# Optimization experiments

Hardware: AMD Instinct MI355X
Metric: run time of the kernel (lower is better)

Reference implementation:

```python
import jax, jax.numpy as jnp
import numpy as np

H, DK, DV, SEG, D = 16, 64, 64, 512, 1024


def setup_inputs() -> dict:
    key = jax.random.key(0)
    ks = jax.random.split(key, 6)
    B, T = 2, 8192
    x = jax.random.normal(ks[0], (B, T, D), jnp.float32)
    Wq = jax.random.normal(ks[1], (H * DK, D), jnp.float32) * 0.02
    Wk = jax.random.normal(ks[2], (H * DK, D), jnp.float32) * 0.02
    Wv = jax.random.normal(ks[3], (H * DV, D), jnp.float32) * 0.02
    Wout = jax.random.normal(ks[4], (D, H * DV), jnp.float32) * 0.02
    betas = jax.random.normal(ks[5], (1, H, 1, DV), jnp.float32)
    return {"x": x, "Wq": Wq, "Wk": Wk, "Wv": Wv, "Wout": Wout, "betas": betas}


def reference(x, Wq, Wk, Wv, Wout, betas):
    B, T, _ = x.shape
    n_seg = T // SEG
    # Projections for the whole sequence, then PyTorch-style .view head split:
    # per segment, (B, SEG, H*dk).view(B, H, SEG, dk) is a raw row-major reshape.
    q = (x @ Wq.T).reshape(B, n_seg, H, SEG, DK)
    k = (x @ Wk.T).reshape(B, n_seg, H, SEG, DK)
    v = (x @ Wv.T).reshape(B, n_seg, H, SEG, DV)
    qs = jnp.moveaxis(q, 1, 0)  # (n_seg, B, H, SEG, DK)
    ks_ = jnp.moveaxis(k, 1, 0)
    vs = jnp.moveaxis(v, 1, 0)

    gate = jax.nn.sigmoid(betas)                 # (1, H, 1, DV)
    scale = 1.0 / jnp.sqrt(jnp.float32(DK))

    mem0 = jnp.zeros((B, H, DK, DV), x.dtype)
    # z broadcasts from (B,H,DV,1) to (B,H,DV,DK) on first update; start dense.
    z0 = jnp.zeros((B, H, DV, DK), x.dtype)

    def step(carry, seg):
        mem, z = carry
        q, k, v = seg
        sq = jax.nn.elu(q) + 1.0                 # (B,H,S,DK)
        sk = jax.nn.elu(k) + 1.0
        z = z + sk.sum(axis=-2, keepdims=True)   # (B,H,DV,DK) via broadcast
        scores = jnp.einsum('bhsd,bhtd->bhst', q, k) * scale
        att_dot = jnp.einsum('bhst,bhtv->bhsv', jax.nn.softmax(scores, axis=-1), v)
        att_mem = jnp.einsum('bhsd,bhdv->bhsv', sq, mem) / jnp.einsum('bhsd,bhdv->bhsv', sq, z)
        mem = mem + jnp.einsum('bhsd,bhsv->bhdv', sk, v)  # linear update (after att_mem)
        att = gate * att_mem + (1.0 - gate) * att_dot     # (B,H,S,DV)
        # PyTorch .view(B, SEG, H*DV) on (B,H,S,DV): raw reshape, no transpose.
        y = att.reshape(B, SEG, H * DV) @ Wout.T          # (B,SEG,D)
        return (mem, z), y

    (_, _), ys = jax.lax.scan(step, (mem0, z0), (qs, ks_, vs))
    out = jnp.moveaxis(ys, 0, 1).reshape(B, T, D)
    return out
```

## Files before the change

kernel.cpp:

```cpp
#include <hip/hip_runtime.h>


#define H_ 16
#define SEG_ 512
#define NSEG_ 16
#define B_ 2
#define T_ 8192
#define D_ 1024
#define BT_ 16384

#define NPROJ ((size_t)BT_ * D_)
#define NW ((size_t)D_ * D_)

__device__ unsigned short g_qb[NPROJ], g_kb[NPROJ], g_vb[NPROJ];
__device__ unsigned short g_xh[NPROJ];
__device__ unsigned short g_wqkv[3 * NW];
__device__ unsigned short g_ath[NPROJ], g_atl[NPROJ];
__device__ unsigned short g_woh[NW], g_wol[NW];
__device__ unsigned short g_vt[(size_t)512 * 64 * 512];
__device__ float g_M[(size_t)512 * 4096];
__device__ float g_z[(size_t)512 * 64];

typedef __attribute__((ext_vector_type(8))) short short8;
typedef __attribute__((ext_vector_type(8))) unsigned short ushort8;
typedef __attribute__((ext_vector_type(4))) float f32x4;

__device__ __forceinline__ float elu1(float x) {
    return x > 0.f ? x + 1.f : __expf(x);
}
__device__ __forceinline__ unsigned short f2bf(float x) {
    unsigned u = __float_as_uint(x);
    u += 0x7fffu + ((u >> 16) & 1u);
    return (unsigned short)(u >> 16);
}
__device__ __forceinline__ float bf2f(unsigned short h) {
    return __uint_as_float((unsigned)h << 16);
}
__device__ __forceinline__ void load_lds16(const unsigned short* g, unsigned short* l) {
    __builtin_amdgcn_global_load_lds(
        (const __attribute__((address_space(1))) unsigned int*)g,
        (__attribute__((address_space(3))) unsigned int*)l, 16, 0, 0);
}
__device__ __forceinline__ int sz8(int row, int blk) {
    return row * 64 + ((blk ^ (row & 7)) << 3);
}

__global__ __launch_bounds__(256) void prep_cast(
    const float* __restrict__ x, const float* __restrict__ Wq,
    const float* __restrict__ Wk, const float* __restrict__ Wv,
    const float* __restrict__ Wout,
    unsigned short* __restrict__ xh, unsigned short* __restrict__ wqkv,
    unsigned short* __restrict__ woh, unsigned short* __restrict__ wol)
{
    const int b = blockIdx.x;
    const int nXB = (int)(NPROJ / 1024);
    const int nWB = (int)(NW / 1024);
    if (b < nXB + 3 * nWB) {
        const float* in;
        unsigned short* out;
        int i;
        if (b < nXB) {
            in = x; out = xh; i = (b * 256 + threadIdx.x) * 4;
        } else {
            const int wsel = (b - nXB) / nWB;
            const int wb   = (b - nXB) % nWB;
            in  = wsel == 0 ? Wq : (wsel == 1 ? Wk : Wv);
            out = wqkv + (size_t)wsel * NW;
            i = (wb * 256 + threadIdx.x) * 4;
        }
        float4 v = *(const float4*)(in + i);
        ushort4 h;
        h.x = f2bf(v.x); h.y = f2bf(v.y); h.z = f2bf(v.z); h.w = f2bf(v.w);
        *(ushort4*)(out + i) = h;
    } else {
        const int wb = b - nXB - 3 * nWB;
        const int i = (wb * 256 + threadIdx.x) * 4;
        float4 v = *(const float4*)(Wout + i);
        ushort4 h, l;
        h.x = f2bf(v.x); l.x = f2bf(v.x - bf2f(h.x));
        h.y = f2bf(v.y); l.y = f2bf(v.y - bf2f(h.y));
        h.z = f2bf(v.z); l.z = f2bf(v.z - bf2f(h.z));
        h.w = f2bf(v.w); l.w = f2bf(v.w - bf2f(h.w));
        *(ushort4*)(woh + i) = h;
        *(ushort4*)(wol + i) = l;
    }
}


#define VMC(N) asm volatile("s_waitcnt vmcnt(" #N ")" ::: "memory")

#define STAGE_A(p, h, tt, u) \
    load_lds16(Aw + ((h) * 128 + (u) * 8) * 1024 + (tt) * 64, \
               &lds[(p) * 32768 + ((h) * 128 + w * 16 + (u) * 8) * 64])
#define STAGE_B(p, h, tt, u) \
    load_lds16(Bww + ((h) * 128 + (u) * 8) * 1024 + (tt) * 64, \
               &lds[(p) * 32768 + 16384 + ((h) * 128 + w * 16 + (u) * 8) * 64])
#define STAGE_AH(p, h, tt) do { STAGE_A(p, h, tt, 0); STAGE_A(p, h, tt, 1); } while (0)
#define STAGE_BH(p, h, tt) do { STAGE_B(p, h, tt, 0); STAGE_B(p, h, tt, 1); } while (0)

#define LDA(PBUF, MLO) do { \
    _Pragma("unroll") for (int m2 = 0; m2 < 4; ++m2) \
    _Pragma("unroll") for (int ks2 = 0; ks2 < 2; ++ks2) \
        a[m2][ks2] = *(const short8*)&lds[(PBUF) * 32768 + aoff[ks2] + ((MLO) + m2) * 1024]; \
} while (0)

#define LDB(PBUF) do { \
    _Pragma("unroll") for (int n2 = 0; n2 < 4; ++n2) \
    _Pragma("unroll") for (int ks2 = 0; ks2 < 2; ++ks2) \
        b[n2][ks2] = *(const short8*)&lds[(PBUF) * 32768 + boff[ks2] + n2 * 1024]; \
} while (0)

#define MFMA_QUAD(MLO, NLO) do { \
    _Pragma("unroll") for (int m2 = 0; m2 < 4; ++m2) \
    _Pragma("unroll") for (int n2 = 0; n2 < 2; ++n2) \
    _Pragma("unroll") for (int ks2 = 0; ks2 < 2; ++ks2) \
        acc[(MLO) + m2][(NLO) + n2] = __builtin_amdgcn_mfma_f32_16x16x32_bf16( \
            a[m2][ks2], b[(NLO) + n2][ks2], acc[(MLO) + m2][(NLO) + n2], 0, 0, 0); \
} while (0)

#define PH(MLO, NLO) do { \
    __builtin_amdgcn_s_barrier(); \
    asm volatile("s_waitcnt lgkmcnt(0)" ::: "memory"); \
    __builtin_amdgcn_sched_barrier(0); \
    __builtin_amdgcn_s_setprio(1); \
    MFMA_QUAD(MLO, NLO); \
    __builtin_amdgcn_s_setprio(0); \
    __builtin_amdgcn_sched_barrier(0); \
    __builtin_amdgcn_s_barrier(); \
} while (0)

__global__ __launch_bounds__(512, 2) void gemm_qkv8(
    const unsigned short* __restrict__ A, const unsigned short* __restrict__ Bw,
    unsigned short* __restrict__ Q, unsigned short* __restrict__ Kp,
    unsigned short* __restrict__ V)
{
    __shared__ unsigned short lds[65536];
    const int t = threadIdx.x, lane = t & 63, w = t >> 6;
    const int wave_m = w >> 2, wave_n = w & 3;

    const int bid = blockIdx.x;
    const int sb = (bid & 7) * 96 + (bid >> 3);
    const int mb = sb / 12, nb = sb % 12;
    const int m0 = mb * 256, n0 = nb * 256;

    const int lrow = lane >> 3;
    const int lcol = ((lane & 7) ^ lrow) * 8;
    const unsigned short* Aw  = A  + (size_t)(m0 + w * 16 + lrow) * 1024 + lcol;
    const unsigned short* Bww = Bw + (size_t)(n0 + w * 16 + lrow) * 1024 + lcol;

    const int fr = lane & 15, g4 = lane >> 4;
    int aoff[2], boff[2];
#pragma unroll
    for (int ks2 = 0; ks2 < 2; ++ks2) {
        aoff[ks2] = (wave_m * 128 + fr) * 64 + (((ks2 * 4 + g4) ^ (fr & 7)) * 8);
        boff[ks2] = 16384 + (wave_n * 64 + fr) * 64 + (((ks2 * 4 + g4) ^ (fr & 7)) * 8);
    }

    f32x4 acc[8][4];
#pragma unroll
    for (int i = 0; i < 8; ++i)
#pragma unroll
        for (int j = 0; j < 4; ++j) acc[i][j] = (f32x4)0.f;
    short8 a[4][2], b[4][2];

    STAGE_BH(0, 0, 0); STAGE_BH(0, 1, 0); STAGE_AH(0, 0, 0); STAGE_AH(0, 1, 0);
    STAGE_BH(1, 0, 1); STAGE_BH(1, 1, 1); STAGE_AH(1, 0, 1);
    VMC(6);
    __builtin_amdgcn_s_barrier();

#pragma unroll 1
    for (int it = 0; it < 7; ++it) {
        const int t1 = 2 * it + 1, t2 = 2 * it + 2, t3 = 2 * it + 3;
        LDB(0); LDA(0, 0);
        STAGE_AH(1, 1, t1);
        PH(0, 0);
        STAGE_BH(0, 0, t2);
        PH(0, 2);
        LDA(0, 4);
        STAGE_BH(0, 1, t2);
        PH(4, 0);
        STAGE_AH(0, 0, t2);
        VMC(6);
        PH(4, 2);
        LDB(1); LDA(1, 0);
        STAGE_AH(0, 1, t2);
        PH(0, 0);
        STAGE_BH(1, 0, t3);
        PH(0, 2);
        LDA(1, 4);
        STAGE_BH(1, 1, t3);
        PH(4, 0);
        STAGE_AH(1, 0, t3);
        VMC(6);
        PH(4, 2);
    }
    LDB(0); LDA(0, 0);
    STAGE_AH(1, 1, 15);
    PH(0, 0);
    PH(0, 2);
    LDA(0, 4);
    PH(4, 0);
    VMC(0);
    PH(4, 2);
    LDB(1); LDA(1, 0);
    PH(0, 0);
    PH(0, 2);
    LDA(1, 4);
    PH(4, 0);
    PH(4, 2);

    const int ccol = lane & 15, crow = (lane >> 4) * 4;
#pragma unroll
    for (int m = 0; m < 8; ++m)
#pragma unroll
        for (int n = 0; n < 4; ++n) {
            const int col = wave_n * 64 + n * 16 + ccol;
            const int cb = col >> 3, cl = col & 7;
#pragma unroll
            for (int r = 0; r < 4; ++r) {
                const int row = wave_m * 128 + m * 16 + crow + r;
                lds[row * 256 + ((cb ^ (row & 31)) << 3) + cl] = f2bf(acc[m][n][r]);
            }
        }
    __syncthreads();
    const int which = n0 >> 10, col0 = n0 & 1023;
    unsigned short* outp = which == 0 ? Q : (which == 1 ? Kp : V);
    const int orow = t >> 1, och = (t & 1) * 128;
    unsigned short* gp = outp + (size_t)(m0 + orow) * 1024 + col0 + och;
#pragma unroll
    for (int u = 0; u < 128; u += 8) {
        const int bo = (och + u) >> 3;
        *(ushort8*)(gp + u) = *(const ushort8*)&lds[orow * 256 + ((bo ^ (orow & 31)) << 3)];
    }
}


#define OSTG(p, arrp, aroff, tt, u) \
    load_lds16(arrp + (size_t)(u) * 16 * 1024 + (tt) * 32, \
               &lds[(p) * 32768 + (aroff) + (w * 32 + (u) * 16) * 32])
#define OUNIT(p, arrp, aroff, tt) do { OSTG(p, arrp, aroff, tt, 0); OSTG(p, arrp, aroff, tt, 1); } while (0)

#define OLDA(PBUF, MLO) do { \
    _Pragma("unroll") for (int m2 = 0; m2 < 4; ++m2) { \
        ah[m2] = *(const short8*)&lds[(PBUF) * 32768 +         ao + ((MLO) + m2) * 512]; \
        al[m2] = *(const short8*)&lds[(PBUF) * 32768 +  8192 + ao + ((MLO) + m2) * 512]; \
    } \
} while (0)

#define OLDB(PBUF) do { \
    _Pragma("unroll") for (int n2 = 0; n2 < 4; ++n2) { \
        bh[n2] = *(const short8*)&lds[(PBUF) * 32768 + 16384 + bo + n2 * 512]; \
        bl[n2] = *(const short8*)&lds[(PBUF) * 32768 + 24576 + bo + n2 * 512]; \
    } \
} while (0)

#define OQUAD(MLO, NLO) do { \
    _Pragma("unroll") for (int m2 = 0; m2 < 4; ++m2) \
    _Pragma("unroll") for (int n2 = 0; n2 < 2; ++n2) { \
        acc[(MLO) + m2][(NLO) + n2] = __builtin_amdgcn_mfma_f32_16x16x32_bf16( \
            ah[m2], bh[(NLO) + n2], acc[(MLO) + m2][(NLO) + n2], 0, 0, 0); \
        acc[(MLO) + m2][(NLO) + n2] = __builtin_amdgcn_mfma_f32_16x16x32_bf16( \
            al[m2], bh[(NLO) + n2], acc[(MLO) + m2][(NLO) + n2], 0, 0, 0); \
        acc[(MLO) + m2][(NLO) + n2] = __builtin_amdgcn_mfma_f32_16x16x32_bf16( \
            ah[m2], bl[(NLO) + n2], acc[(MLO) + m2][(NLO) + n2], 0, 0, 0); \
    } \
} while (0)

#define OPH(MLO, NLO) do { \
    __builtin_amdgcn_s_barrier(); \
    asm volatile("s_waitcnt lgkmcnt(0)" ::: "memory"); \
    __builtin_amdgcn_sched_barrier(0); \
    __builtin_amdgcn_s_setprio(1); \
    OQUAD(MLO, NLO); \
    __builtin_amdgcn_s_setprio(0); \
    __builtin_amdgcn_sched_barrier(0); \
    __builtin_amdgcn_s_barrier(); \
} while (0)

__global__ __launch_bounds__(512, 2) void gemm_bt8(
    const unsigned short* __restrict__ Ah, const unsigned short* __restrict__ Al,
    const unsigned short* __restrict__ Bh, const unsigned short* __restrict__ Bl,
    float* __restrict__ C)
{
    __shared__ unsigned short lds[65536];
    const int t = threadIdx.x, lane = t & 63, w = t >> 6;
    const int wave_m = w >> 2, wave_n = w & 3;

    const int bid = blockIdx.x;
    const int sb = (bid & 7) * 32 + (bid >> 3);
    const int m0 = (sb >> 2) * 256, n0 = (sb & 3) * 256;

    const int lrow = lane >> 2;
    const int lcol = ((lane & 3) ^ ((lane >> 3) & 3)) * 8;
    const unsigned short* Ahp = Ah + (size_t)(m0 + w * 32 + lrow) * 1024 + lcol;
    const unsigned short* Alp = Al + (size_t)(m0 + w * 32 + lrow) * 1024 + lcol;
    const unsigned short* Bhp = Bh + (size_t)(n0 + w * 32 + lrow) * 1024 + lcol;
    const unsigned short* Blp = Bl + (size_t)(n0 + w * 32 + lrow) * 1024 + lcol;

    const int fr = lane & 15, g4 = lane >> 4;
    const int xo = (g4 ^ ((fr >> 1) & 3)) * 8;
    const int ao = (wave_m * 128 + fr) * 32 + xo;
    const int bo = (wave_n * 64 + fr) * 32 + xo;

    f32x4 acc[8][4];
#pragma unroll
    for (int i = 0; i < 8; ++i)
#pragma unroll
        for (int j = 0; j < 4; ++j) acc[i][j] = (f32x4)0.f;
    short8 ah[4], al[4], bh[4], bl[4];

    OUNIT(0, Bhp, 16384, 0); OUNIT(0, Blp, 24576, 0); OUNIT(0, Ahp, 0, 0); OUNIT(0, Alp, 8192, 0);
    OUNIT(1, Bhp, 16384, 1); OUNIT(1, Blp, 24576, 1); OUNIT(1, Ahp, 0, 1);
    VMC(6);
    __builtin_amdgcn_s_barrier();

#pragma unroll 1
    for (int it = 0; it < 15; ++it) {
        const int t1 = 2 * it + 1, t2 = 2 * it + 2, t3 = 2 * it + 3;
        OLDB(0); OLDA(0, 0);
        OUNIT(1, Alp, 8192, t1);
        OPH(0, 0);
        OUNIT(0, Bhp, 16384, t2);
        OPH(0, 2);
        OLDA(0, 4);
        OUNIT(0, Blp, 24576, t2);
        OPH(4, 0);
        OUNIT(0, Ahp, 0, t2);
        VMC(6);
        OPH(4, 2);
        OLDB(1); OLDA(1, 0);
        OUNIT(0, Alp, 8192, t2);
        OPH(0, 0);
        OUNIT(1, Bhp, 16384, t3);
        OPH(0, 2);
        OLDA(1, 4);
        OUNIT(1, Blp, 24576, t3);
        OPH(4, 0);
        OUNIT(1, Ahp, 0, t3);
        VMC(6);
        OPH(4, 2);
    }
    OLDB(0); OLDA(0, 0);
    OUNIT(1, Alp, 8192, 31);
    OPH(0, 0);
    OPH(0, 2);
    OLDA(0, 4);
    OPH(4, 0);
    VMC(0);
    OPH(4, 2);
    OLDB(1); OLDA(1, 0);
    OPH(0, 0);
    OPH(0, 2);
    OLDA(1, 4);
    OPH(4, 0);
    OPH(4, 2);

    const int ccol = lane & 15, crow = (lane >> 4) * 4;
#pragma unroll
    for (int m = 0; m < 8; ++m)
#pragma unroll
        for (int n = 0; n < 4; ++n) {
            float* cp = C + (size_t)(m0 + wave_m * 128 + m * 16 + crow) * 1024
                          + (n0 + wave_n * 64 + n * 16 + ccol);
#pragma unroll
            for (int r = 0; r < 4; ++r) cp[(size_t)r * 1024] = acc[m][n][r];
        }
}

__global__ __launch_bounds__(256) void seg_stats(
    const unsigned short* __restrict__ kproj, const unsigned short* __restrict__ vproj,
    float* __restrict__ Mseg, float* __restrict__ zsum,
    unsigned short* __restrict__ vtg)
{
    __shared__ unsigned short sm_kh[64 * 64];
    __shared__ unsigned short sm_kl[64 * 64];
    __shared__ unsigned short sm_vt[64 * 64];
    const int idx = blockIdx.x;
    const int seg = idx & 15;
    const int bh  = idx >> 4;
    const int h   = bh & 15;
    const int b   = bh >> 4;
    const size_t base = ((size_t)b * T_ + (size_t)seg * SEG_ + (size_t)h * 32) * D_;
    const unsigned short* kt = kproj + base;
    const unsigned short* vt = vproj + base;
    const int t    = threadIdx.x;
    const int lane = t & 63;
    const int w    = t >> 6;
    const int c16  = lane & 15;
    const int g4   = lane >> 4;
    const int lr   = t >> 2;
    const int lc   = (t & 3) * 16;

    short8 bones;
#pragma unroll
    for (int j = 0; j < 8; ++j) bones[j] = (short)0x3F80;

    f32x4 acc[4];
#pragma unroll
    for (int nt = 0; nt < 4; ++nt) acc[nt] = (f32x4)0.f;
    f32x4 zacc = (f32x4)0.f;

    for (int c0 = 0; c0 < SEG_; c0 += 64) {
        __syncthreads();
        {
            const int row = c0 + lane;
            const unsigned short* kp = kt + (size_t)row * 64 + w * 16;
            const unsigned short* vp = vt + (size_t)row * 64 + w * 16;
            ushort8 k0 = *(const ushort8*)kp, k1 = *(const ushort8*)(kp + 8);
            ushort8 v0 = *(const ushort8*)vp, v1 = *(const ushort8*)(vp + 8);
            const int tb = lane >> 3, tl = lane & 7;
#pragma unroll
            for (int e = 0; e < 8; ++e) {
                const float f0 = elu1(bf2f(k0[e]));
                const unsigned short h0 = f2bf(f0), l0 = f2bf(f0 - bf2f(h0));
                const float f1 = elu1(bf2f(k1[e]));
                const unsigned short h1 = f2bf(f1), l1 = f2bf(f1 - bf2f(h1));
                const int a0 = sz8(w * 16 + e,     tb) + tl;
                const int a1 = sz8(w * 16 + 8 + e, tb) + tl;
                sm_kh[a0] = h0; sm_kl[a0] = l0; sm_vt[a0] = v0[e];
                sm_kh[a1] = h1; sm_kl[a1] = l1; sm_vt[a1] = v1[e];
            }
        }
        __syncthreads();
#pragma unroll
        for (int ks = 0; ks < 2; ++ks) {
            const short8 ahh = *(const short8*)&sm_kh[sz8(w * 16 + c16, ks * 4 + g4)];
            const short8 alo = *(const short8*)&sm_kl[sz8(w * 16 + c16, ks * 4 + g4)];
            zacc = __builtin_amdgcn_mfma_f32_16x16x32_bf16(ahh, bones, zacc, 0, 0, 0);
            zacc = __builtin_amdgcn_mfma_f32_16x16x32_bf16(alo, bones, zacc, 0, 0, 0);
#pragma unroll
            for (int nt = 0; nt < 4; ++nt) {
                const short8 bv = *(const short8*)&sm_vt[sz8(nt * 16 + c16, ks * 4 + g4)];
                acc[nt] = __builtin_amdgcn_mfma_f32_16x16x32_bf16(ahh, bv, acc[nt], 0, 0, 0);
                acc[nt] = __builtin_amdgcn_mfma_f32_16x16x32_bf16(alo, bv, acc[nt], 0, 0, 0);
            }
        }
        {
            unsigned short* vo = vtg + ((size_t)idx * 64 + lr) * 512 + c0 + lc;
            *(ushort8*)vo       = *(const ushort8*)&sm_vt[sz8(lr, lc >> 3)];
            *(ushort8*)(vo + 8) = *(const ushort8*)&sm_vt[sz8(lr, (lc >> 3) + 1)];
        }
    }
    float* Mout = Mseg + (size_t)idx * 4096;
#pragma unroll
    for (int nt = 0; nt < 4; ++nt)
#pragma unroll
        for (int r = 0; r < 4; ++r)
            Mout[(size_t)(w * 16 + g4 * 4 + r) * 64 + nt * 16 + c16] = acc[nt][r];
    if (c16 == 0) {
#pragma unroll
        for (int r = 0; r < 4; ++r)
            zsum[(size_t)idx * 64 + w * 16 + g4 * 4 + r] = zacc[r];
    }
}

__global__ __launch_bounds__(256) void prefix_scan(
    float* __restrict__ M, float* __restrict__ z)
{
    const int blk = blockIdx.x;
    const int bh  = blk >> 2, sl = blk & 3;
    const int t   = threadIdx.x;
    const size_t off = (size_t)bh * NSEG_ * 4096 + (size_t)sl * 1024 + (size_t)t * 4;
    float4 run = make_float4(0.f, 0.f, 0.f, 0.f);
    float runz = 0.f;
    for (int seg = 0; seg < NSEG_; ++seg) {
        const size_t o = off + (size_t)seg * 4096;
        float4 m = *(const float4*)(M + o);
        *(float4*)(M + o) = run;
        run.x += m.x; run.y += m.y; run.z += m.z; run.w += m.w;
        if (sl == 0 && t < 64) {
            const size_t oz = ((size_t)bh * NSEG_ + seg) * 64 + t;
            runz += z[oz];
            z[oz] = runz;
        }
    }
}

__global__ __launch_bounds__(512) void attn_mfma(
    const unsigned short* __restrict__ qproj, const unsigned short* __restrict__ kproj,
    const unsigned short* __restrict__ vtg, const float* __restrict__ memb,
    const float* __restrict__ Zaf, const float* __restrict__ betas,
    unsigned short* __restrict__ ath, unsigned short* __restrict__ atl)
{
    __shared__ unsigned short smK[8 * 4096];
    __shared__ unsigned short smV[8 * 4096];
    __shared__ unsigned short smM[4096];
    __shared__ unsigned short smP[128 * 64];
    __shared__ float Zsh[64], gsh[64];

    const int rest = blockIdx.x;
    const int bh   = rest >> 4;
    const int seg  = rest & 15;
    const int h    = bh & 15;
    const int b    = bh >> 4;
    const size_t base = ((size_t)b * T_ + (size_t)seg * SEG_ + (size_t)h * 32) * D_;

    const int t    = threadIdx.x;
    const int lane = t & 63;
    const int w    = t >> 6;
    const int c16  = lane & 15;
    const int g4   = lane >> 4;
    const int sr   = t >> 3;
    const int sg   = t & 7;

    const unsigned short* qt = qproj + base;
    const unsigned short* kt = kproj + base;
    const unsigned short* vt = vtg + (size_t)rest * (64 * 512);
    const float* mb = memb + (size_t)rest * 4096;

    if (t < 64) {
        Zsh[t] = Zaf[(size_t)rest * 64 + t];
        gsh[t] = 1.f / (1.f + __expf(-betas[h * 64 + t]));
    }

    {
        const float* mp = mb + (size_t)sr * 64 + sg * 8;
#pragma unroll
        for (int u = 0; u < 2; ++u) {
            float4 m4 = *(const float4*)(mp + u * 4);
            smM[sz8(sg * 8 + u * 4 + 0, sr >> 3) + (sr & 7)] = f2bf(m4.x);
            smM[sz8(sg * 8 + u * 4 + 1, sr >> 3) + (sr & 7)] = f2bf(m4.y);
            smM[sz8(sg * 8 + u * 4 + 2, sr >> 3) + (sr & 7)] = f2bf(m4.z);
            smM[sz8(sg * 8 + u * 4 + 3, sr >> 3) + (sr & 7)] = f2bf(m4.w);
        }
    }
#pragma unroll
    for (int kb = 0; kb < 8; ++kb) {
        *(ushort8*)&smK[kb * 4096 + sz8(sr, sg)] =
            *(const ushort8*)(kt + (size_t)(kb * 64 + sr) * 64 + sg * 8);
        *(ushort8*)&smV[kb * 4096 + sz8(sr, sg)] =
            *(const ushort8*)(vt + (size_t)sr * 512 + kb * 64 + sg * 8);
    }
    __syncthreads();

    short8 bones;
#pragma unroll
    for (int j = 0; j < 8; ++j) bones[j] = (short)0x3F80;

#pragma unroll 1
    for (int qc2 = 0; qc2 < 4; ++qc2) {
        short8 qh[2], sqh[2];
        float rowsum = 0.f;
#pragma unroll
        for (int ks = 0; ks < 2; ++ks) {
            const unsigned short* qp =
                qt + (size_t)(qc2 * 128 + w * 16 + c16) * 64 + g4 * 8 + ks * 32;
            ushort8 qv = *(const ushort8*)qp;
            short8 qf, sf;
#pragma unroll
            for (int j = 0; j < 8; ++j) {
                float e = elu1(bf2f(qv[j]));
                rowsum += e;
                qf[j] = (short)qv[j];
                sf[j] = (short)f2bf(e);
            }
            qh[ks] = qf; sqh[ks] = sf;
        }
        rowsum += __shfl_xor(rowsum, 16);
        rowsum += __shfl_xor(rowsum, 32);

        f32x4 numf[4];
#pragma unroll
        for (int nf = 0; nf < 4; ++nf) numf[nf] = (f32x4)0.f;
#pragma unroll
        for (int ks = 0; ks < 2; ++ks)
#pragma unroll
            for (int nf = 0; nf < 4; ++nf) {
                short8 bm = *(const short8*)&smM[sz8(nf * 16 + c16, g4 + ks * 4)];
                numf[nf] = __builtin_amdgcn_mfma_f32_16x16x32_bf16(sqh[ks], bm, numf[nf], 0, 0, 0);
            }

        f32x4 o[4];
#pragma unroll
        for (int nf = 0; nf < 4; ++nf) o[nf] = (f32x4)0.f;
        float mrow[4] = {-1e30f, -1e30f, -1e30f, -1e30f};
        float lrow[4] = {0.f, 0.f, 0.f, 0.f};

#pragma unroll 1
        for (int kb = 0; kb < 8; ++kb) {
            f32x4 s[4];
#pragma unroll
            for (int nf = 0; nf < 4; ++nf) s[nf] = (f32x4)0.f;
#pragma unroll
            for (int ks = 0; ks < 2; ++ks)
#pragma unroll
                for (int nf = 0; nf < 4; ++nf) {
                    short8 bk = *(const short8*)&smK[kb * 4096 + sz8(nf * 16 + c16, g4 + ks * 4)];
                    s[nf] = __builtin_amdgcn_mfma_f32_16x16x32_bf16(qh[ks], bk, s[nf], 0, 0, 0);
                }
#pragma unroll
            for (int nf = 0; nf < 4; ++nf) s[nf] *= 0.125f;

            float pmax[4];
#pragma unroll
            for (int r = 0; r < 4; ++r)
                pmax[r] = fmaxf(fmaxf(s[0][r], s[1][r]), fmaxf(s[2][r], s[3][r]));
            const bool ok = pmax[0] <= mrow[0] + 8.f && pmax[1] <= mrow[1] + 8.f &&
                            pmax[2] <= mrow[2] + 8.f && pmax[3] <= mrow[3] + 8.f;
            if (!__all(ok)) {
#pragma unroll
                for (int r = 0; r < 4; ++r) {
                    float mx = pmax[r];
                    mx = fmaxf(mx, __shfl_xor(mx, 1));
                    mx = fmaxf(mx, __shfl_xor(mx, 2));
                    mx = fmaxf(mx, __shfl_xor(mx, 4));
                    mx = fmaxf(mx, __shfl_xor(mx, 8));
                    const float mnew = fmaxf(mrow[r], mx);
                    const float corr = __expf(mrow[r] - mnew);
                    mrow[r] = mnew;
                    lrow[r] *= corr;
#pragma unroll
                    for (int nf = 0; nf < 4; ++nf) o[nf][r] *= corr;
                }
            }
#pragma unroll
            for (int nf = 0; nf < 4; ++nf)
#pragma unroll
                for (int r = 0; r < 4; ++r) {
                    s[nf][r] = __expf(s[nf][r] - mrow[r]);
                    smP[sz8(w * 16 + g4 * 4 + r, nf * 2 + (c16 >> 3)) + (c16 & 7)] =
                        f2bf(s[nf][r]);
                }

            f32x4 psum = (f32x4)0.f;
#pragma unroll
            for (int ks = 0; ks < 2; ++ks) {
                short8 pa = *(const short8*)&smP[sz8(w * 16 + c16, g4 + ks * 4)];
                psum = __builtin_amdgcn_mfma_f32_16x16x32_bf16(pa, bones, psum, 0, 0, 0);
#pragma unroll
                for (int nf = 0; nf < 4; ++nf) {
                    short8 bv = *(const short8*)&smV[kb * 4096 + sz8(nf * 16 + c16, g4 + ks * 4)];
                    o[nf] = __builtin_amdgcn_mfma_f32_16x16x32_bf16(pa, bv, o[nf], 0, 0, 0);
                }
            }
#pragma unroll
            for (int r = 0; r < 4; ++r) lrow[r] += psum[r];
        }

        float rs[4], invl[4];
#pragma unroll
        for (int r = 0; r < 4; ++r) {
            rs[r]   = __shfl(rowsum, (g4 << 2) + r);
            invl[r] = 1.f / lrow[r];
        }
        float res[4][4];
#pragma unroll
        for (int nf = 0; nf < 4; ++nf) {
            const int col = nf * 16 + c16;
            const float Zc = Zsh[col], gc = gsh[col];
            const float izc = 1.f / Zc;
#pragma unroll
            for (int r = 0; r < 4; ++r) {
                const float adot = o[nf][r] * invl[r];
                const float amem = numf[nf][r] * izc / rs[r];
                res[nf][r] = gc * amem + (1.f - gc) * adot;
            }
        }
        const int orow = t >> 2, olc = (t & 3) * 16;
        const size_t ob = base + (size_t)(qc2 * 128 + orow) * 64 + olc;
#pragma unroll
        for (int nf = 0; nf < 4; ++nf)
#pragma unroll
            for (int r = 0; r < 4; ++r)
                smP[sz8(w * 16 + g4 * 4 + r, nf * 2 + (c16 >> 3)) + (c16 & 7)] =
                    f2bf(res[nf][r]);
        __syncthreads();
        *(ushort8*)(ath + ob)     = *(const ushort8*)&smP[sz8(orow, olc >> 3)];
        *(ushort8*)(ath + ob + 8) = *(const ushort8*)&smP[sz8(orow, (olc >> 3) + 1)];
        __syncthreads();
#pragma unroll
        for (int nf = 0; nf < 4; ++nf)
#pragma unroll
            for (int r = 0; r < 4; ++r) {
                const unsigned short hv = f2bf(res[nf][r]);
                smP[sz8(w * 16 + g4 * 4 + r, nf * 2 + (c16 >> 3)) + (c16 & 7)] =
                    f2bf(res[nf][r] - bf2f(hv));
            }
        __syncthreads();
        *(ushort8*)(atl + ob)     = *(const ushort8*)&smP[sz8(orow, olc >> 3)];
        *(ushort8*)(atl + ob + 8) = *(const ushort8*)&smP[sz8(orow, (olc >> 3) + 1)];
        __syncthreads();
    }
}

extern "C" void kernel_launch(void* const* d_in, const int* in_sizes, int n_in,
                              void* d_out, int out_size, void* d_ws, size_t ws_size,
                              hipStream_t stream) {
    const float* x     = (const float*)d_in[0];
    const float* Wq    = (const float*)d_in[1];
    const float* Wk    = (const float*)d_in[2];
    const float* Wv    = (const float*)d_in[3];
    const float* Wout  = (const float*)d_in[4];
    const float* betas = (const float*)d_in[5];
    float* out = (float*)d_out;
    (void)d_ws; (void)ws_size;

    float *M, *z;
    unsigned short *qb, *kb, *vb, *xh, *wqkv, *vt, *ath, *atl, *woh, *wol;
    hipGetSymbolAddress((void**)&qb,   HIP_SYMBOL(g_qb));
    hipGetSymbolAddress((void**)&kb,   HIP_SYMBOL(g_kb));
    hipGetSymbolAddress((void**)&vb,   HIP_SYMBOL(g_vb));
    hipGetSymbolAddress((void**)&xh,   HIP_SYMBOL(g_xh));
    hipGetSymbolAddress((void**)&wqkv, HIP_SYMBOL(g_wqkv));
    hipGetSymbolAddress((void**)&vt,   HIP_SYMBOL(g_vt));
    hipGetSymbolAddress((void**)&ath,  HIP_SYMBOL(g_ath));
    hipGetSymbolAddress((void**)&atl,  HIP_SYMBOL(g_atl));
    hipGetSymbolAddress((void**)&woh,  HIP_SYMBOL(g_woh));
    hipGetSymbolAddress((void**)&wol,  HIP_SYMBOL(g_wol));
    hipGetSymbolAddress((void**)&M,    HIP_SYMBOL(g_M));
    hipGetSymbolAddress((void**)&z,    HIP_SYMBOL(g_z));

    const int nXB = (int)(NPROJ / 1024), nWB = (int)(NW / 1024);
    prep_cast<<<nXB + 4 * nWB, 256, 0, stream>>>(x, Wq, Wk, Wv, Wout,
                                                 xh, wqkv, woh, wol);

    gemm_qkv8<<<dim3(768), 512, 0, stream>>>(xh, wqkv, qb, kb, vb);
    seg_stats<<<B_ * H_ * NSEG_, 256, 0, stream>>>(kb, vb, M, z, vt);
    prefix_scan<<<B_ * H_ * 4, 256, 0, stream>>>(M, z);
    attn_mfma<<<B_ * H_ * NSEG_, 512, 0, stream>>>(qb, kb, vt, M, z, betas, ath, atl);
    gemm_bt8<<<dim3(256), 512, 0, stream>>>(ath, atl, woh, wol, out);
}
```

Measured before the change: 483.7 us.

## Halve QKV GEMM LDS tile K-depth to raise occupancy and split epilogue

Cuts the QKV projection GEMM's per-stage K slice from 64 to 32, which halves LDS use from 128KB to 64KB and doubles the main-loop iteration count. Launch bounds rise from 2 to 4 blocks per CU, and the epilogue writes the 256-row output tile in two 128-row halves so it fits the smaller LDS. The goal is more resident blocks to hide latency, at the cost of more barriers and shallower prefetch per stage. The output GEMM's shared array is renamed with no functional change.

```diff
diff --git a/kernel.cpp b/kernel.cpp
--- a/kernel.cpp
+++ b/kernel.cpp
@@ -89,33 +89,28 @@
 
 #define VMC(N) asm volatile("s_waitcnt vmcnt(" #N ")" ::: "memory")
 
-#define STAGE_A(p, h, tt, u) \
-    load_lds16(Aw + ((h) * 128 + (u) * 8) * 1024 + (tt) * 64, \
-               &lds[(p) * 32768 + ((h) * 128 + w * 16 + (u) * 8) * 64])
-#define STAGE_B(p, h, tt, u) \
-    load_lds16(Bww + ((h) * 128 + (u) * 8) * 1024 + (tt) * 64, \
-               &lds[(p) * 32768 + 16384 + ((h) * 128 + w * 16 + (u) * 8) * 64])
-#define STAGE_AH(p, h, tt) do { STAGE_A(p, h, tt, 0); STAGE_A(p, h, tt, 1); } while (0)
-#define STAGE_BH(p, h, tt) do { STAGE_B(p, h, tt, 0); STAGE_B(p, h, tt, 1); } while (0)
+#define QSTG_A(p, u, tt) \
+    load_lds16(Aw + (size_t)(u) * 128 * 1024 + (tt) * 32, \
+               &lds[(p) * 16384 + (u) * 4096 + w * 512])
+#define QSTG_B(p, u, tt) \
+    load_lds16(Bww + (size_t)(u) * 128 * 1024 + (tt) * 32, \
+               &lds[(p) * 16384 + 8192 + (u) * 4096 + w * 512])
 
 #define LDA(PBUF, MLO) do { \
     _Pragma("unroll") for (int m2 = 0; m2 < 4; ++m2) \
-    _Pragma("unroll") for (int ks2 = 0; ks2 < 2; ++ks2) \
-        a[m2][ks2] = *(const short8*)&lds[(PBUF) * 32768 + aoff[ks2] + ((MLO) + m2) * 1024]; \
+        a[m2] = *(const short8*)&lds[(PBUF) * 16384 + aoff + ((MLO) + m2) * 512]; \
 } while (0)
 
 #define LDB(PBUF) do { \
     _Pragma("unroll") for (int n2 = 0; n2 < 4; ++n2) \
-    _Pragma("unroll") for (int ks2 = 0; ks2 < 2; ++ks2) \
-        b[n2][ks2] = *(const short8*)&lds[(PBUF) * 32768 + boff[ks2] + n2 * 1024]; \
+        b[n2] = *(const short8*)&lds[(PBUF) * 16384 + boff + n2 * 512]; \
 } while (0)
 
 #define MFMA_QUAD(MLO, NLO) do { \
     _Pragma("unroll") for (int m2 = 0; m2 < 4; ++m2) \
     _Pragma("unroll") for (int n2 = 0; n2 < 2; ++n2) \
-    _Pragma("unroll") for (int ks2 = 0; ks2 < 2; ++ks2) \
         acc[(MLO) + m2][(NLO) + n2] = __builtin_amdgcn_mfma_f32_16x16x32_bf16( \
-            a[m2][ks2], b[(NLO) + n2][ks2], acc[(MLO) + m2][(NLO) + n2], 0, 0, 0); \
+            a[m2], b[(NLO) + n2], acc[(MLO) + m2][(NLO) + n2], 0, 0, 0); \
 } while (0)
 
 #define PH(MLO, NLO) do { \
@@ -129,12 +124,12 @@
     __builtin_amdgcn_s_barrier(); \
 } while (0)
 
-__global__ __launch_bounds__(512, 2) void gemm_qkv8(
+__global__ __launch_bounds__(512, 4) void gemm_qkv8(
     const unsigned short* __restrict__ A, const unsigned short* __restrict__ Bw,
     unsigned short* __restrict__ Q, unsigned short* __restrict__ Kp,
     unsigned short* __restrict__ V)
 {
-    __shared__ unsigned short lds[65536];
+    __shared__ unsigned short lds[32768];
     const int t = threadIdx.x, lane = t & 63, w = t >> 6;
     const int wave_m = w >> 2, wave_n = w & 3;
 
@@ -143,59 +138,56 @@
     const int mb = sb / 12, nb = sb % 12;
     const int m0 = mb * 256, n0 = nb * 256;
 
-    const int lrow = lane >> 3;
-    const int lcol = ((lane & 7) ^ lrow) * 8;
-    const unsigned short* Aw  = A  + (size_t)(m0 + w * 16 + lrow) * 1024 + lcol;
-    const unsigned short* Bww = Bw + (size_t)(n0 + w * 16 + lrow) * 1024 + lcol;
+    const int lrow = lane >> 2;
+    const int scol = ((lane & 3) ^ ((lrow >> 1) & 3)) * 8;
+    const unsigned short* Aw  = A  + (size_t)(m0 + w * 16 + lrow) * 1024 + scol;
+    const unsigned short* Bww = Bw + (size_t)(n0 + w * 16 + lrow) * 1024 + scol;
 
     const int fr = lane & 15, g4 = lane >> 4;
-    int aoff[2], boff[2];
-#pragma unroll
-    for (int ks2 = 0; ks2 < 2; ++ks2) {
-        aoff[ks2] = (wave_m * 128 + fr) * 64 + (((ks2 * 4 + g4) ^ (fr & 7)) * 8);
-        boff[ks2] = 16384 + (wave_n * 64 + fr) * 64 + (((ks2 * 4 + g4) ^ (fr & 7)) * 8);
-    }
+    const int xo = (g4 ^ ((fr >> 1) & 3)) * 8;
+    const int aoff = (wave_m * 128 + fr) * 32 + xo;
+    const int boff = 8192 + (wave_n * 64 + fr) * 32 + xo;
 
     f32x4 acc[8][4];
 #pragma unroll
     for (int i = 0; i < 8; ++i)
 #pragma unroll
         for (int j = 0; j < 4; ++j) acc[i][j] = (f32x4)0.f;
-    short8 a[4][2], b[4][2];
-
-    STAGE_BH(0, 0, 0); STAGE_BH(0, 1, 0); STAGE_AH(0, 0, 0); STAGE_AH(0, 1, 0);
-    STAGE_BH(1, 0, 1); STAGE_BH(1, 1, 1); STAGE_AH(1, 0, 1);
-    VMC(6);
+    short8 a[4], b[4];
+
+    QSTG_B(0, 0, 0); QSTG_B(0, 1, 0); QSTG_A(0, 0, 0); QSTG_A(0, 1, 0);
+    QSTG_B(1, 0, 1); QSTG_B(1, 1, 1); QSTG_A(1, 0, 1);
+    VMC(3);
     __builtin_amdgcn_s_barrier();
 
 #pragma unroll 1
-    for (int it = 0; it < 7; ++it) {
+    for (int it = 0; it < 15; ++it) {
         const int t1 = 2 * it + 1, t2 = 2 * it + 2, t3 = 2 * it + 3;
         LDB(0); LDA(0, 0);
-        STAGE_AH(1, 1, t1);
+        QSTG_A(1, 1, t1);
         PH(0, 0);
-        STAGE_BH(0, 0, t2);
+        QSTG_B(0, 0, t2);
         PH(0, 2);
         LDA(0, 4);
-        STAGE_BH(0, 1, t2);
+        QSTG_B(0, 1, t2);
         PH(4, 0);
-        STAGE_AH(0, 0, t2);
-        VMC(6);
+        QSTG_A(0, 0, t2);
+        VMC(3);
         PH(4, 2);
         LDB(1); LDA(1, 0);
-        STAGE_AH(0, 1, t2);
+        QSTG_A(0, 1, t2);
         PH(0, 0);
-        STAGE_BH(1, 0, t3);
+        QSTG_B(1, 0, t3);
         PH(0, 2);
         LDA(1, 4);
-        STAGE_BH(1, 1, t3);
+        QSTG_B(1, 1, t3);
         PH(4, 0);
-        STAGE_AH(1, 0, t3);
-        VMC(6);
+        QSTG_A(1, 0, t3);
+        VMC(3);
         PH(4, 2);
     }
     LDB(0); LDA(0, 0);
-    STAGE_AH(1, 1, 15);
+    QSTG_A(1, 1, 31);
     PH(0, 0);
     PH(0, 2);
     LDA(0, 4);
@@ -210,47 +202,53 @@
     PH(4, 2);
 
     const int ccol = lane & 15, crow = (lane >> 4) * 4;
-#pragma unroll
-    for (int m = 0; m < 8; ++m)
-#pragma unroll
-        for (int n = 0; n < 4; ++n) {
-            const int col = wave_n * 64 + n * 16 + ccol;
-            const int cb = col >> 3, cl = col & 7;
-#pragma unroll
-            for (int r = 0; r < 4; ++r) {
-                const int row = wave_m * 128 + m * 16 + crow + r;
-                lds[row * 256 + ((cb ^ (row & 31)) << 3) + cl] = f2bf(acc[m][n][r]);
-            }
-        }
-    __syncthreads();
     const int which = n0 >> 10, col0 = n0 & 1023;
     unsigned short* outp = which == 0 ? Q : (which == 1 ? Kp : V);
-    const int orow = t >> 1, och = (t & 1) * 128;
-    unsigned short* gp = outp + (size_t)(m0 + orow) * 1024 + col0 + och;
-#pragma unroll
-    for (int u = 0; u < 128; u += 8) {
-        const int bo = (och + u) >> 3;
-        *(ushort8*)(gp + u) = *(const ushort8*)&lds[orow * 256 + ((bo ^ (orow & 31)) << 3)];
+    const int orow = t >> 2, och = (t & 3) * 64;
+#pragma unroll 1
+    for (int half = 0; half < 2; ++half) {
+        __syncthreads();
+        if (wave_m == half) {
+#pragma unroll
+            for (int m = 0; m < 8; ++m)
+#pragma unroll
+                for (int n = 0; n < 4; ++n) {
+                    const int col = wave_n * 64 + n * 16 + ccol;
+                    const int cb = col >> 3, cl = col & 7;
+#pragma unroll
+                    for (int r = 0; r < 4; ++r) {
+                        const int row = m * 16 + crow + r;
+                        lds[row * 256 + ((cb ^ (row & 31)) << 3) + cl] = f2bf(acc[m][n][r]);
+                    }
+                }
+        }
+        __syncthreads();
+        unsigned short* gp = outp + (size_t)(m0 + half * 128 + orow) * 1024 + col0 + och;
+#pragma unroll
+        for (int u = 0; u < 64; u += 8) {
+            const int bo = (och + u) >> 3;
+            *(ushort8*)(gp + u) = *(const ushort8*)&lds[orow * 256 + ((bo ^ (orow & 31)) << 3)];
+        }
     }
 }
 
 
 #define OSTG(p, arrp, aroff, tt, u) \
     load_lds16(arrp + (size_t)(u) * 16 * 1024 + (tt) * 32, \
-               &lds[(p) * 32768 + (aroff) + (w * 32 + (u) * 16) * 32])
+               &olds[(p) * 32768 + (aroff) + (w * 32 + (u) * 16) * 32])
 #define OUNIT(p, arrp, aroff, tt) do { OSTG(p, arrp, aroff, tt, 0); OSTG(p, arrp, aroff, tt, 1); } while (0)
 
 #define OLDA(PBUF, MLO) do { \
     _Pragma("unroll") for (int m2 = 0; m2 < 4; ++m2) { \
-        ah[m2] = *(const short8*)&lds[(PBUF) * 32768 +         ao + ((MLO) + m2) * 512]; \
-        al[m2] = *(const short8*)&lds[(PBUF) * 32768 +  8192 + ao + ((MLO) + m2) * 512]; \
+        ah[m2] = *(const short8*)&olds[(PBUF) * 32768 +         ao + ((MLO) + m2) * 512]; \
+        al[m2] = *(const short8*)&olds[(PBUF) * 32768 +  8192 + ao + ((MLO) + m2) * 512]; \
     } \
 } while (0)
 
 #define OLDB(PBUF) do { \
     _Pragma("unroll") for (int n2 = 0; n2 < 4; ++n2) { \
-        bh[n2] = *(const short8*)&lds[(PBUF) * 32768 + 16384 + bo + n2 * 512]; \
-        bl[n2] = *(const short8*)&lds[(PBUF) * 32768 + 24576 + bo + n2 * 512]; \
+        bh[n2] = *(const short8*)&olds[(PBUF) * 32768 + 16384 + bo + n2 * 512]; \
+        bl[n2] = *(const short8*)&olds[(PBUF) * 32768 + 24576 + bo + n2 * 512]; \
     } \
 } while (0)
 
@@ -282,7 +280,7 @@
     const unsigned short* __restrict__ Bh, const unsigned short* __restrict__ Bl,
     float* __restrict__ C)
 {
-    __shared__ unsigned short lds[65536];
+    __shared__ unsigned short olds[65536];
     const int t = threadIdx.x, lane = t & 63, w = t >> 6;
     const int wave_m = w >> 2, wave_n = w & 3;
 
```

After: 1.775 ms. 3.67x slower.
